# Kernel tuning notes

Hardware: AMD Instinct MI355X
Metric: run time of the kernel (lower is better)

## Reference

```python
import jax, jax.numpy as jnp
import numpy as np

A = 9          # num anchors per location
C = 256        # feature channels
H = W = 32     # feature map size
B = 1          # batch (module's squeeze_-based NMS implies batch=1)
N = A * H * W  # total proposals
IOU_THR = 0.9
EPS = 1e-5     # BatchNorm eps
NEG_SLOPE = 0.01  # LeakyReLU default


def setup_inputs() -> dict:
    key = jax.random.key(0)
    ks = jax.random.split(key, 8)
    inp = {
        "x": jax.random.normal(ks[0], (B, C, H, W), dtype=jnp.float32),
        "anchors": jax.random.uniform(ks[1], (A, 4), dtype=jnp.float32),
        # depthwise 3x3 conv (groups=C): torch weight shape [C,1,3,3]
        "dw_w": jax.random.normal(ks[2], (C, 1, 3, 3), dtype=jnp.float32) * 0.05,
        # pointwise 1x1 conv [C_out, C_in]
        "pw_w": jax.random.normal(ks[3], (C, C), dtype=jnp.float32) * 0.05,
        "bn1_gamma": jnp.ones((C,), jnp.float32),
        "bn1_beta": jnp.zeros((C,), jnp.float32),
        "bn1_mean": jnp.zeros((C,), jnp.float32),
        "bn1_var": jnp.ones((C,), jnp.float32),
        # anchors_conv: 1x1 conv 256 -> 4A, BN, ReLU6
        "anc_w": jax.random.normal(ks[4], (4 * A, C), dtype=jnp.float32) * 0.05,
        "anc_gamma": jnp.ones((4 * A,), jnp.float32),
        "anc_beta": jnp.zeros((4 * A,), jnp.float32),
        "anc_mean": jnp.zeros((4 * A,), jnp.float32),
        "anc_var": jnp.ones((4 * A,), jnp.float32),
        # objectness_conv: 1x1 conv 256 -> A, BN, Sigmoid
        "obj_w": jax.random.normal(ks[5], (A, C), dtype=jnp.float32) * 0.05,
        "obj_gamma": jnp.ones((A,), jnp.float32),
        "obj_beta": jnp.zeros((A,), jnp.float32),
        "obj_mean": jnp.zeros((A,), jnp.float32),
        "obj_var": jnp.ones((A,), jnp.float32),
    }
    return inp


def _bn(h, gamma, beta, mean, var):
    # inference-mode BatchNorm2d over channel dim 1 of [B,C,H,W]
    inv = jax.lax.rsqrt(var + EPS)
    return (h - mean[None, :, None, None]) * (inv * gamma)[None, :, None, None] + beta[None, :, None, None]


def _nms_keep(boxes, scores, thr):
    # greedy NMS (torchvision semantics, boxes as x1,y1,x2,y2) -> bool keep mask in original order
    order = jnp.argsort(-scores)
    b = boxes[order]  # [N,4] sorted by score desc
    x1, y1, x2, y2 = b[:, 0], b[:, 1], b[:, 2], b[:, 3]
    areas = (x2 - x1) * (y2 - y1)
    ix1 = jnp.maximum(x1[:, None], x1[None, :])
    iy1 = jnp.maximum(y1[:, None], y1[None, :])
    ix2 = jnp.minimum(x2[:, None], x2[None, :])
    iy2 = jnp.minimum(y2[:, None], y2[None, :])
    inter = jnp.clip(ix2 - ix1, 0.0) * jnp.clip(iy2 - iy1, 0.0)
    iou = inter / (areas[:, None] + areas[None, :] - inter)
    idx = jnp.arange(boxes.shape[0])

    def body(i, keep):
        sup = (iou[i] > thr) & (idx > i) & keep[i]
        return keep & ~sup

    keep_sorted = jax.lax.fori_loop(0, boxes.shape[0], body, jnp.ones((boxes.shape[0],), bool))
    return jnp.zeros((boxes.shape[0],), bool).at[order].set(keep_sorted)


def reference(x, anchors, dw_w, pw_w, bn1_gamma, bn1_beta, bn1_mean, bn1_var,
              anc_w, anc_gamma, anc_beta, anc_mean, anc_var,
              obj_w, obj_gamma, obj_beta, obj_mean, obj_var):
    batch = x.shape[0]
    hw = x.shape[2] * x.shape[3]
    # DepthSeparableConv2d: depthwise 3x3 (groups=C) + pointwise 1x1
    h = jax.lax.conv_general_dilated(
        x, dw_w, window_strides=(1, 1), padding=((1, 1), (1, 1)),
        dimension_numbers=("NCHW", "OIHW", "NCHW"), feature_group_count=C)
    h = jnp.einsum("bchw,oc->bohw", h, pw_w)
    h = jax.nn.leaky_relu(_bn(h, bn1_gamma, bn1_beta, bn1_mean, bn1_var), NEG_SLOPE)
    # heads
    anc = jnp.einsum("bchw,oc->bohw", h, anc_w)
    anc = jnp.clip(_bn(anc, anc_gamma, anc_beta, anc_mean, anc_var), 0.0, 6.0)  # ReLU6
    obj = jnp.einsum("bchw,oc->bohw", h, obj_w)
    obj = jax.nn.sigmoid(_bn(obj, obj_gamma, obj_beta, obj_mean, obj_var))
    # anchor decode
    corr = anc.reshape(batch, A, 4, hw)              # [B,A,4,HW]
    anch = anchors.reshape(1, A, 4, 1)
    pos = corr[:, :, :2, :] + anch[:, :, :2, :]
    size = jnp.exp(corr[:, :, 2:, :]) * anch[:, :, 2:, :]
    corrected = jnp.concatenate([pos, size], axis=2)  # [B,A,4,HW]
    boxes = corrected.transpose(0, 2, 1, 3).reshape(batch, 4, -1).transpose(0, 2, 1)  # [B,N,4]
    scores = obj.reshape(batch, A, 1, hw).transpose(0, 2, 1, 3).reshape(batch, 1, -1).transpose(0, 2, 1)  # [B,N,1]
    boxes = boxes[0]          # squeeze_ (batch==1)
    scores = scores[0, :, 0]
    keep = _nms_keep(boxes, scores, IOU_THR)
    m = jax.lax.stop_gradient(keep.astype(boxes.dtype))
    # fixed-shape equivalent of index_select: suppressed rows zeroed
    return jnp.concatenate([boxes * m[:, None], (scores * m)[:, None]], axis=1)  # [N,5]
```

## Files before the change

kernel.cpp:

```cpp
#include <hip/hip_runtime.h>
#include <hip/hip_bf16.h>

#define EPSF 1e-5f
#define IOU_THRF 0.9f
#define NBOX 9216
#define NWORDS 144
#define CAND_CAP 4096
#define FIRE_CAP 1024
#define NTILES 666

__global__ __launch_bounds__(256) void dw_conv(const float* __restrict__ x,
                                               const float* __restrict__ w,
                                               float* __restrict__ h0) {
    int idx = blockIdx.x * 256 + threadIdx.x;
    int c = idx >> 10, p = idx & 1023;
    int yy = p >> 5, xx = p & 31;
    const float* xi = x + (c << 10);
    const float* wc = w + c * 9;
    float acc = 0.f;
    #pragma unroll
    for (int dy = -1; dy <= 1; ++dy) {
        int y2 = yy + dy;
        if ((unsigned)y2 >= 32u) continue;
        #pragma unroll
        for (int dx = -1; dx <= 1; ++dx) {
            int x2 = xx + dx;
            if ((unsigned)x2 >= 32u) continue;
            acc += wc[(dy + 1) * 3 + (dx + 1)] * xi[y2 * 32 + x2];
        }
    }
    h0[idx] = acc;
}

__global__ __launch_bounds__(256) void pw_conv(const float* __restrict__ h0,
                                               const float* __restrict__ w,
                                               const float* __restrict__ g,
                                               const float* __restrict__ b,
                                               const float* __restrict__ mu,
                                               const float* __restrict__ var,
                                               float* __restrict__ h1) {
    int p = blockIdx.x * 256 + threadIdx.x;
    int o0 = blockIdx.y * 4;
    float acc0 = 0.f, acc1 = 0.f, acc2 = 0.f, acc3 = 0.f;
    for (int c = 0; c < 256; ++c) {
        float hv = h0[(c << 10) + p];
        acc0 += w[(o0 + 0) * 256 + c] * hv;
        acc1 += w[(o0 + 1) * 256 + c] * hv;
        acc2 += w[(o0 + 2) * 256 + c] * hv;
        acc3 += w[(o0 + 3) * 256 + c] * hv;
    }
    float accs[4] = {acc0, acc1, acc2, acc3};
    #pragma unroll
    for (int k = 0; k < 4; ++k) {
        int o = o0 + k;
        float inv = 1.0f / sqrtf(var[o] + EPSF);
        float v = (accs[k] - mu[o]) * (inv * g[o]) + b[o];
        v = (v >= 0.f) ? v : 0.01f * v;
        h1[(o << 10) + p] = v;
    }
}

__global__ __launch_bounds__(256) void heads(const float* __restrict__ h1,
                                             const float* __restrict__ anc_w,
                                             const float* __restrict__ ag,
                                             const float* __restrict__ ab,
                                             const float* __restrict__ am,
                                             const float* __restrict__ av,
                                             const float* __restrict__ obj_w,
                                             const float* __restrict__ og,
                                             const float* __restrict__ ob,
                                             const float* __restrict__ om,
                                             const float* __restrict__ ov,
                                             const float* __restrict__ anchors,
                                             float* __restrict__ boxes,
                                             float* __restrict__ scores) {
    int p = blockIdx.x * 256 + threadIdx.x;
    int o = blockIdx.y;
    const float* wrow = (o < 36) ? (anc_w + o * 256) : (obj_w + (o - 36) * 256);
    float acc = 0.f;
    for (int c = 0; c < 256; ++c) acc += wrow[c] * h1[(c << 10) + p];
    if (o < 36) {
        float inv = 1.0f / sqrtf(av[o] + EPSF);
        float v = (acc - am[o]) * (inv * ag[o]) + ab[o];
        v = fminf(fmaxf(v, 0.f), 6.f);
        int a = o >> 2, k = o & 3;
        float anch = anchors[a * 4 + k];
        float val = (k < 2) ? (v + anch) : (expf(v) * anch);
        boxes[(size_t)(a * 1024 + p) * 4 + k] = val;
    } else {
        int a = o - 36;
        float inv = 1.0f / sqrtf(ov[a] + EPSF);
        float v = (acc - om[a]) * (inv * og[a]) + ob[a];
        scores[a * 1024 + p] = 1.0f / (1.0f + expf(-v));
    }
}

__global__ __launch_bounds__(256) void rank_partial(const float* __restrict__ scores,
                                                    unsigned* __restrict__ rank) {
    __shared__ float4 sm[288];
    int mbase = blockIdx.y * 1152;
    for (int t = threadIdx.x; t < 288; t += 256)
        sm[t] = ((const float4*)(scores + mbase))[t];
    __syncthreads();
    int n = blockIdx.x * 256 + threadIdx.x;
    float s = scores[n];
    unsigned cnt = 0;
    for (int q = 0; q < 288; ++q) {
        float4 v = sm[q];
        int m = mbase + q * 4;
        cnt += (v.x > s) || (v.x == s && (m + 0) < n);
        cnt += (v.y > s) || (v.y == s && (m + 1) < n);
        cnt += (v.z > s) || (v.z == s && (m + 2) < n);
        cnt += (v.w > s) || (v.w == s && (m + 3) < n);
    }
    atomicAdd(&rank[n], cnt);
}

__global__ __launch_bounds__(256) void scatter_sorted(const float* __restrict__ boxes,
                                                      const unsigned* __restrict__ rank,
                                                      int* __restrict__ order,
                                                      float* __restrict__ sboxes,
                                                      float* __restrict__ sareas) {
    int n = blockIdx.x * 256 + threadIdx.x;
    unsigned r = rank[n];
    order[r] = n;
    float4 bx = ((const float4*)boxes)[n];
    ((float4*)sboxes)[r] = bx;
    sareas[r] = (bx.z - bx.x) * (bx.w - bx.y);
}

__global__ __launch_bounds__(256) void cand_detect(const float* __restrict__ sboxes,
                                                   const float* __restrict__ sareas,
                                                   unsigned long long* __restrict__ rnz64) {
    __shared__ float CX1[256], CY1[256], CX2[256], CY2[256], CAR[256];
    int rem = blockIdx.x, rb = 0;
    while (rem >= 36 - rb) { rem -= 36 - rb; ++rb; }
    int s = rb + rem;
    int tid = threadIdx.x;
    int i = rb * 256 + tid;
    {
        int j = s * 256 + tid;
        float4 cb = ((const float4*)sboxes)[j];
        CX1[tid] = cb.x; CY1[tid] = cb.y; CX2[tid] = cb.z; CY2[tid] = cb.w;
        CAR[tid] = sareas[j];
    }
    __syncthreads();
    float4 b = ((const float4*)sboxes)[i];
    float ar = sareas[i];
    bool any = false;

    if (s == rb) {
        for (int idx = tid + 1; idx < 256; ++idx) {
            float ix = fminf(b.z, CX2[idx]) - fmaxf(b.x, CX1[idx]);
            float iy = fminf(b.w, CY2[idx]) - fmaxf(b.y, CY1[idx]);
            float inter = fmaxf(ix, 0.f) * fmaxf(iy, 0.f);
            float denom = ar + CAR[idx] - inter;
            if (inter > 0.85f * denom) {
                if (inter / denom > IOU_THRF) any = true;
            }
        }
    } else {
        const float4* X1v = (const float4*)CX1;
        const float4* Y1v = (const float4*)CY1;
        const float4* X2v = (const float4*)CX2;
        const float4* Y2v = (const float4*)CY2;
        const float4* ARv = (const float4*)CAR;
        #pragma unroll 2
        for (int q = 0; q < 64; ++q) {
            float4 x1 = X1v[q], y1 = Y1v[q], x2 = X2v[q], y2 = Y2v[q], aa = ARv[q];
            #define CCHK(k) { \
                float ix = fminf(b.z, x2.k) - fmaxf(b.x, x1.k); \
                float iy = fminf(b.w, y2.k) - fmaxf(b.y, y1.k); \
                float inter = fmaxf(ix, 0.f) * fmaxf(iy, 0.f);  \
                float denom = ar + aa.k - inter;                \
                if (inter > 0.85f * denom) {                    \
                    if (inter / denom > IOU_THRF) any = true;   \
                } }
            CCHK(x) CCHK(y) CCHK(z) CCHK(w)
            #undef CCHK
        }
    }
    unsigned long long bal = __ballot(any);
    if ((tid & 63) == 0) atomicOr(&rnz64[rb * 4 + (tid >> 6)], bal);
}

__global__ __launch_bounds__(64) void compact_cand(const unsigned long long* __restrict__ rnz64,
                                                   const float* __restrict__ sboxes,
                                                   const float* __restrict__ sareas,
                                                   int* __restrict__ cidx,
                                                   float4* __restrict__ cboxes,
                                                   float* __restrict__ carea,
                                                   int* __restrict__ knum) {
    int lane = threadIdx.x;
    int base = 0;
    for (int w = 0; w < NWORDS; ++w) {
        unsigned long long bits = rnz64[w];
        if (bits & (1ull << lane)) {
            int pos = base + (int)__popcll(bits & ((1ull << lane) - 1ull));
            if (pos < CAND_CAP) {
                int i = w * 64 + lane;
                cidx[pos] = i;
                cboxes[pos] = ((const float4*)sboxes)[i];
                carea[pos] = sareas[i];
            }
        }
        base += (int)__popcll(bits);
    }
    if (lane == 0) knum[0] = base < CAND_CAP ? base : CAND_CAP;
}

__global__ __launch_bounds__(256) void gate_build(const float4* __restrict__ cboxes,
                                                  const float* __restrict__ carea,
                                                  const int* __restrict__ knum,
                                                  unsigned long long* __restrict__ gate) {
    int Kc = knum[0];
    int a = blockIdx.x * 4 + (threadIdx.x >> 6);
    int w = threadIdx.x & 63;
    if (a >= Kc) return;
    float4 b = cboxes[a];
    float ar = carea[a];
    unsigned long long bits = 0ull;
    int cbase = w * 64;
    if (cbase < Kc) {
        int lim = Kc - cbase; if (lim > 64) lim = 64;
        for (int t = 0; t < lim; ++t) {
            int c = cbase + t;
            if (c > a) {
                float4 cb = cboxes[c];
                float ix = fminf(b.z, cb.z) - fmaxf(b.x, cb.x);
                float iy = fminf(b.w, cb.w) - fmaxf(b.y, cb.y);
                float inter = fmaxf(ix, 0.f) * fmaxf(iy, 0.f);
                float denom = ar + carea[c] - inter;
                if (inter > 0.85f * denom) {
                    if (inter / denom > IOU_THRF) bits |= (1ull << t);
                }
            }
        }
    }
    gate[(size_t)a * 64 + w] = bits;
}

__device__ inline unsigned long long rdl64(unsigned long long v, int l) {
    unsigned lo = (unsigned)__builtin_amdgcn_readlane((int)(unsigned)(v & 0xffffffffull), l);
    unsigned hi = (unsigned)__builtin_amdgcn_readlane((int)(unsigned)(v >> 32), l);
    return ((unsigned long long)hi << 32) | lo;
}

__global__ __launch_bounds__(64) void nms_scan2(const unsigned long long* __restrict__ gate,
                                                const int* __restrict__ knum,
                                                int* __restrict__ fire_ord,
                                                int* __restrict__ fire_cnt) {
    int lane = threadIdx.x;
    int Kc = knum[0];
    int nw = (Kc + 63) >> 6;
    unsigned long long sup = 0ull;
    int nf = 0;
    for (int w = 0; w < nw; ++w) {
        int rem = Kc - w * 64;
        unsigned long long mskw = (rem >= 64) ? ~0ull : ((1ull << rem) - 1ull);
        unsigned long long alive = ~rdl64(sup, w) & mskw;
        while (alive) {
            unsigned long long snap = alive;
            int t0 = __builtin_ctzll(snap); snap &= snap - 1;
            int t1 = -1, t2 = -1, t3 = -1, t4 = -1, t5 = -1, t6 = -1, t7 = -1;
            if (snap) { t1 = __builtin_ctzll(snap); snap &= snap - 1; }
            if (snap) { t2 = __builtin_ctzll(snap); snap &= snap - 1; }
            if (snap) { t3 = __builtin_ctzll(snap); snap &= snap - 1; }
            if (snap) { t4 = __builtin_ctzll(snap); snap &= snap - 1; }
            if (snap) { t5 = __builtin_ctzll(snap); snap &= snap - 1; }
            if (snap) { t6 = __builtin_ctzll(snap); snap &= snap - 1; }
            if (snap) { t7 = __builtin_ctzll(snap); snap &= snap - 1; }
            int u1 = t1 < 0 ? t0 : t1, u2 = t2 < 0 ? t0 : t2, u3 = t3 < 0 ? t0 : t3;
            int u4 = t4 < 0 ? t0 : t4, u5 = t5 < 0 ? t0 : t5, u6 = t6 < 0 ? t0 : t6;
            int u7 = t7 < 0 ? t0 : t7;
            size_t wb = (size_t)(w << 6);
            unsigned long long g0 = gate[(wb + t0) * 64 + lane];
            unsigned long long g1 = gate[(wb + u1) * 64 + lane];
            unsigned long long g2 = gate[(wb + u2) * 64 + lane];
            unsigned long long g3 = gate[(wb + u3) * 64 + lane];
            unsigned long long g4 = gate[(wb + u4) * 64 + lane];
            unsigned long long g5 = gate[(wb + u5) * 64 + lane];
            unsigned long long g6 = gate[(wb + u6) * 64 + lane];
            unsigned long long g7 = gate[(wb + u7) * 64 + lane];
            #define PROC(tk, gk) \
                if (tk >= 0 && ((alive >> tk) & 1ull)) { \
                    if (lane == 0 && nf < FIRE_CAP) fire_ord[nf] = (w << 6) + tk; \
                    ++nf; sup |= gk; \
                    alive &= ~(1ull << tk); \
                    alive &= ~rdl64(gk, w); \
                }
            PROC(t0, g0) PROC(t1, g1) PROC(t2, g2) PROC(t3, g3)
            PROC(t4, g4) PROC(t5, g5) PROC(t6, g6) PROC(t7, g7)
            #undef PROC
        }
    }
    if (lane == 0) fire_cnt[0] = nf < FIRE_CAP ? nf : FIRE_CAP;
}

__global__ __launch_bounds__(256) void finalize(const float* __restrict__ sboxes,
                                                const float* __restrict__ sareas,
                                                const float* __restrict__ scores,
                                                const int* __restrict__ order,
                                                const float4* __restrict__ cboxes,
                                                const float* __restrict__ carea,
                                                const int* __restrict__ cidx,
                                                const int* __restrict__ fire_ord,
                                                const int* __restrict__ fire_cnt,
                                                float* __restrict__ out) {
    __shared__ float4 FB[FIRE_CAP];
    __shared__ float FA[FIRE_CAP];
    __shared__ int FP[FIRE_CAP];
    int tid = threadIdx.x;
    int fc = fire_cnt[0];
    for (int k = tid; k < fc; k += 256) {
        int o = fire_ord[k];
        FB[k] = cboxes[o];
        FA[k] = carea[o];
        FP[k] = cidx[o];
    }
    __syncthreads();
    int j = blockIdx.x * 256 + tid;
    float4 b = ((const float4*)sboxes)[j];
    float aj = sareas[j];
    bool supp = false;
    for (int k = 0; k < fc; ++k) {
        float4 f = FB[k];
        float ix = fminf(b.z, f.z) - fmaxf(b.x, f.x);
        float iy = fminf(b.w, f.w) - fmaxf(b.y, f.y);
        float inter = fmaxf(ix, 0.f) * fmaxf(iy, 0.f);
        float denom = FA[k] + aj - inter;
        if (FP[k] < j && inter > 0.85f * denom) {
            if (inter / denom > IOU_THRF) supp = true;
        }
    }
    int n = order[j];
    float m = supp ? 0.f : 1.f;
    out[(size_t)n * 5 + 0] = b.x * m;
    out[(size_t)n * 5 + 1] = b.y * m;
    out[(size_t)n * 5 + 2] = b.z * m;
    out[(size_t)n * 5 + 3] = b.w * m;
    out[(size_t)n * 5 + 4] = scores[n] * m;
}

extern "C" void kernel_launch(void* const* d_in, const int* in_sizes, int n_in,
                              void* d_out, int out_size, void* d_ws, size_t ws_size,
                              hipStream_t stream) {
    const float* x      = (const float*)d_in[0];
    const float* anchors= (const float*)d_in[1];
    const float* dw_w   = (const float*)d_in[2];
    const float* pw_w   = (const float*)d_in[3];
    const float* bn1g   = (const float*)d_in[4];
    const float* bn1b   = (const float*)d_in[5];
    const float* bn1m   = (const float*)d_in[6];
    const float* bn1v   = (const float*)d_in[7];
    const float* anc_w  = (const float*)d_in[8];
    const float* ag     = (const float*)d_in[9];
    const float* ab     = (const float*)d_in[10];
    const float* am     = (const float*)d_in[11];
    const float* av     = (const float*)d_in[12];
    const float* obj_w  = (const float*)d_in[13];
    const float* og     = (const float*)d_in[14];
    const float* ob     = (const float*)d_in[15];
    const float* om     = (const float*)d_in[16];
    const float* ov     = (const float*)d_in[17];
    float* out = (float*)d_out;

    char* ws = (char*)d_ws;
    size_t off = 0;
    auto alloc = [&](size_t bytes) -> char* {
        char* p = ws + off;
        off = (off + bytes + 255) & ~(size_t)255;
        return p;
    };
    float* h0      = (float*)alloc(256 * 1024 * 4);
    float* h1      = (float*)alloc(256 * 1024 * 4);
    float* boxes   = (float*)alloc(NBOX * 4 * 4);
    float* scores  = (float*)alloc(NBOX * 4);
    unsigned* rank = (unsigned*)alloc(NBOX * 4);
    int* order     = (int*)alloc(NBOX * 4);
    float* sboxes  = (float*)alloc(NBOX * 4 * 4);
    float* sareas  = (float*)alloc(NBOX * 4);
    unsigned long long* rnz64 = (unsigned long long*)alloc(NWORDS * 8);
    int* cidx      = (int*)alloc(CAND_CAP * 4);
    float4* cboxes = (float4*)alloc(CAND_CAP * 16);
    float* carea   = (float*)alloc(CAND_CAP * 4);
    int* knum      = (int*)alloc(256);
    int* fire_ord  = (int*)alloc(FIRE_CAP * 4);
    int* fire_cnt  = (int*)alloc(256);
    unsigned long long* gate = (unsigned long long*)alloc((size_t)CAND_CAP * 64 * 8);

    hipMemsetAsync(rank, 0, NBOX * 4, stream);
    hipMemsetAsync(rnz64, 0, NWORDS * 8, stream);

    dw_conv<<<1024, 256, 0, stream>>>(x, dw_w, h0);
    pw_conv<<<dim3(4, 64), 256, 0, stream>>>(h0, pw_w, bn1g, bn1b, bn1m, bn1v, h1);
    heads<<<dim3(4, 45), 256, 0, stream>>>(h1, anc_w, ag, ab, am, av,
                                           obj_w, og, ob, om, ov, anchors, boxes, scores);
    rank_partial<<<dim3(36, 8), 256, 0, stream>>>(scores, rank);
    scatter_sorted<<<36, 256, 0, stream>>>(boxes, rank, order, sboxes, sareas);
    cand_detect<<<NTILES, 256, 0, stream>>>(sboxes, sareas, rnz64);
    compact_cand<<<1, 64, 0, stream>>>(rnz64, sboxes, sareas, cidx, cboxes, carea, knum);
    gate_build<<<CAND_CAP / 4, 256, 0, stream>>>(cboxes, carea, knum, gate);
    nms_scan2<<<1, 64, 0, stream>>>(gate, knum, fire_ord, fire_cnt);
    finalize<<<36, 256, 0, stream>>>(sboxes, sareas, scores, order,
                                     cboxes, carea, cidx, fire_ord, fire_cnt, out);
}
```

Baseline: 366.5 us.

## Decouple serial NMS scan from gate loads using diagonal gate blocks and delayed suppression

gate_build now also writes the diagonal and next-diagonal 64-bit gate words per candidate into compact arrays. The serial single-wave scan reads these from registers (prefetched two words ahead) to resolve in-word and next-word suppression. This takes the dependent global gate load off the critical per-keep path. Full gate rows are queued and OR'd into the suppression mask two iterations later, so their load latency is hidden. compact_cand also loads the rnz64 bitmask once into registers and reads words via readlane instead of issuing a broadcast global load per word. The risks are added register pressure, branchy queue handling, and a subtle correctness dependence on the two-word delay.

Measured after the change: 445.7 us. 1.22x slower.

```diff
diff --git a/kernel.cpp b/kernel.cpp
--- a/kernel.cpp
+++ b/kernel.cpp
@@ -184,6 +184,12 @@
     if ((tid & 63) == 0) atomicOr(&rnz64[rb * 4 + (tid >> 6)], bal);
 }
 
+__device__ inline unsigned long long rdl64(unsigned long long v, int l) {
+    unsigned lo = (unsigned)__builtin_amdgcn_readlane((int)(unsigned)(v & 0xffffffffull), l);
+    unsigned hi = (unsigned)__builtin_amdgcn_readlane((int)(unsigned)(v >> 32), l);
+    return ((unsigned long long)hi << 32) | lo;
+}
+
 __global__ __launch_bounds__(64) void compact_cand(const unsigned long long* __restrict__ rnz64,
                                                    const float* __restrict__ sboxes,
                                                    const float* __restrict__ sareas,
@@ -192,9 +198,13 @@
                                                    float* __restrict__ carea,
                                                    int* __restrict__ knum) {
     int lane = threadIdx.x;
+    unsigned long long rz0 = rnz64[lane];
+    unsigned long long rz1 = rnz64[64 + lane];
+    unsigned long long rz2 = rnz64[128 + lane];
     int base = 0;
     for (int w = 0; w < NWORDS; ++w) {
-        unsigned long long bits = rnz64[w];
+        unsigned long long bits = (w < 64) ? rdl64(rz0, w)
+                                : (w < 128) ? rdl64(rz1, w - 64) : rdl64(rz2, w - 128);
         if (bits & (1ull << lane)) {
             int pos = base + (int)__popcll(bits & ((1ull << lane) - 1ull));
             if (pos < CAND_CAP) {
@@ -212,7 +222,9 @@
 __global__ __launch_bounds__(256) void gate_build(const float4* __restrict__ cboxes,
                                                   const float* __restrict__ carea,
                                                   const int* __restrict__ knum,
-                                                  unsigned long long* __restrict__ gate) {
+                                                  unsigned long long* __restrict__ gate,
+                                                  unsigned long long* __restrict__ diag0,
+                                                  unsigned long long* __restrict__ diag1) {
     int Kc = knum[0];
     int a = blockIdx.x * 4 + (threadIdx.x >> 6);
     int w = threadIdx.x & 63;
@@ -238,15 +250,14 @@
         }
     }
     gate[(size_t)a * 64 + w] = bits;
-}
-
-__device__ inline unsigned long long rdl64(unsigned long long v, int l) {
-    unsigned lo = (unsigned)__builtin_amdgcn_readlane((int)(unsigned)(v & 0xffffffffull), l);
-    unsigned hi = (unsigned)__builtin_amdgcn_readlane((int)(unsigned)(v >> 32), l);
-    return ((unsigned long long)hi << 32) | lo;
+    int aw = a >> 6;
+    if (w == aw) diag0[a] = bits;
+    if (w == aw + 1) diag1[a] = bits;
 }
 
 __global__ __launch_bounds__(64) void nms_scan2(const unsigned long long* __restrict__ gate,
+                                                const unsigned long long* __restrict__ diag0,
+                                                const unsigned long long* __restrict__ diag1,
                                                 const int* __restrict__ knum,
                                                 int* __restrict__ fire_ord,
                                                 int* __restrict__ fire_cnt) {
@@ -254,45 +265,48 @@
     int Kc = knum[0];
     int nw = (Kc + 63) >> 6;
     unsigned long long sup = 0ull;
+    unsigned long long carry = 0ull;
     int nf = 0;
+
+    unsigned long long qa0=0,qa1=0,qa2=0,qa3=0,qa4=0,qa5=0,qa6=0,qa7=0; int nA = 0;
+    unsigned long long qb0=0,qb1=0,qb2=0,qb3=0,qb4=0,qb5=0,qb6=0,qb7=0; int nB = 0;
+
+    unsigned long long d0A = diag0[lane], d0B = diag0[64 + lane];
+    unsigned long long d1A = diag1[lane], d1B = diag1[64 + lane];
+
     for (int w = 0; w < nw; ++w) {
-        int rem = Kc - w * 64;
-        unsigned long long mskw = (rem >= 64) ? ~0ull : ((1ull << rem) - 1ull);
-        unsigned long long alive = ~rdl64(sup, w) & mskw;
+        int pf = (w + 2) * 64 + lane;
+        unsigned long long d0C = diag0[pf];
+        unsigned long long d1C = diag1[pf];
+
+        if (nB > 0) { sup |= qb0;
+            if (nB > 1) sup |= qb1; if (nB > 2) sup |= qb2; if (nB > 3) sup |= qb3;
+            if (nB > 4) sup |= qb4; if (nB > 5) sup |= qb5; if (nB > 6) sup |= qb6;
+            if (nB > 7) sup |= qb7; }
+        qb0=qa0; qb1=qa1; qb2=qa2; qb3=qa3; qb4=qa4; qb5=qa5; qb6=qa6; qb7=qa7;
+        nB = nA; nA = 0;
+
+        int rem = Kc - (w << 6);
+        unsigned long long maskw = (rem >= 64) ? ~0ull : ((1ull << rem) - 1ull);
+        unsigned long long alive = ~(rdl64(sup, w) | carry) & maskw;
+        unsigned long long carry_next = 0ull;
+
         while (alive) {
-            unsigned long long snap = alive;
-            int t0 = __builtin_ctzll(snap); snap &= snap - 1;
-            int t1 = -1, t2 = -1, t3 = -1, t4 = -1, t5 = -1, t6 = -1, t7 = -1;
-            if (snap) { t1 = __builtin_ctzll(snap); snap &= snap - 1; }
-            if (snap) { t2 = __builtin_ctzll(snap); snap &= snap - 1; }
-            if (snap) { t3 = __builtin_ctzll(snap); snap &= snap - 1; }
-            if (snap) { t4 = __builtin_ctzll(snap); snap &= snap - 1; }
-            if (snap) { t5 = __builtin_ctzll(snap); snap &= snap - 1; }
-            if (snap) { t6 = __builtin_ctzll(snap); snap &= snap - 1; }
-            if (snap) { t7 = __builtin_ctzll(snap); snap &= snap - 1; }
-            int u1 = t1 < 0 ? t0 : t1, u2 = t2 < 0 ? t0 : t2, u3 = t3 < 0 ? t0 : t3;
-            int u4 = t4 < 0 ? t0 : t4, u5 = t5 < 0 ? t0 : t5, u6 = t6 < 0 ? t0 : t6;
-            int u7 = t7 < 0 ? t0 : t7;
-            size_t wb = (size_t)(w << 6);
-            unsigned long long g0 = gate[(wb + t0) * 64 + lane];
-            unsigned long long g1 = gate[(wb + u1) * 64 + lane];
-            unsigned long long g2 = gate[(wb + u2) * 64 + lane];
-            unsigned long long g3 = gate[(wb + u3) * 64 + lane];
-            unsigned long long g4 = gate[(wb + u4) * 64 + lane];
-            unsigned long long g5 = gate[(wb + u5) * 64 + lane];
-            unsigned long long g6 = gate[(wb + u6) * 64 + lane];
-            unsigned long long g7 = gate[(wb + u7) * 64 + lane];
-            #define PROC(tk, gk) \
-                if (tk >= 0 && ((alive >> tk) & 1ull)) { \
-                    if (lane == 0 && nf < FIRE_CAP) fire_ord[nf] = (w << 6) + tk; \
-                    ++nf; sup |= gk; \
-                    alive &= ~(1ull << tk); \
-                    alive &= ~rdl64(gk, w); \
-                }
-            PROC(t0, g0) PROC(t1, g1) PROC(t2, g2) PROC(t3, g3)
-            PROC(t4, g4) PROC(t5, g5) PROC(t6, g6) PROC(t7, g7)
-            #undef PROC
-        }
+            int t = __builtin_ctzll(alive);
+            if (lane == 0 && nf < FIRE_CAP) fire_ord[nf] = (w << 6) + t;
+            ++nf;
+            unsigned long long g = gate[((size_t)(w << 6) + t) * 64 + lane];
+            if (nA == 0) qa0 = g; else if (nA == 1) qa1 = g; else if (nA == 2) qa2 = g;
+            else if (nA == 3) qa3 = g; else if (nA == 4) qa4 = g; else if (nA == 5) qa5 = g;
+            else if (nA == 6) qa6 = g; else if (nA == 7) qa7 = g;
+            else sup |= g;
+            if (nA < 8) ++nA;
+            alive &= ~(1ull << t);
+            alive &= ~rdl64(d0A, t);
+            carry_next |= rdl64(d1A, t);
+        }
+        carry = carry_next;
+        d0A = d0B; d0B = d0C; d1A = d1B; d1B = d1C;
     }
     if (lane == 0) fire_cnt[0] = nf < FIRE_CAP ? nf : FIRE_CAP;
 }
@@ -380,17 +394,19 @@
     int* order     = (int*)alloc(NBOX * 4);
     float* sboxes  = (float*)alloc(NBOX * 4 * 4);
     float* sareas  = (float*)alloc(NBOX * 4);
-    unsigned long long* rnz64 = (unsigned long long*)alloc(NWORDS * 8);
+    unsigned long long* rnz64 = (unsigned long long*)alloc(192 * 8);
     int* cidx      = (int*)alloc(CAND_CAP * 4);
     float4* cboxes = (float4*)alloc(CAND_CAP * 16);
     float* carea   = (float*)alloc(CAND_CAP * 4);
     int* knum      = (int*)alloc(256);
     int* fire_ord  = (int*)alloc(FIRE_CAP * 4);
     int* fire_cnt  = (int*)alloc(256);
-    unsigned long long* gate = (unsigned long long*)alloc((size_t)CAND_CAP * 64 * 8);
+    unsigned long long* gate  = (unsigned long long*)alloc((size_t)CAND_CAP * 64 * 8);
+    unsigned long long* diag0 = (unsigned long long*)alloc((CAND_CAP + 192) * 8);
+    unsigned long long* diag1 = (unsigned long long*)alloc((CAND_CAP + 192) * 8);
 
     hipMemsetAsync(rank, 0, NBOX * 4, stream);
-    hipMemsetAsync(rnz64, 0, NWORDS * 8, stream);
+    hipMemsetAsync(rnz64, 0, 192 * 8, stream);
 
     dw_conv<<<1024, 256, 0, stream>>>(x, dw_w, h0);
     pw_conv<<<dim3(4, 64), 256, 0, stream>>>(h0, pw_w, bn1g, bn1b, bn1m, bn1v, h1);
@@ -400,8 +416,8 @@
     scatter_sorted<<<36, 256, 0, stream>>>(boxes, rank, order, sboxes, sareas);
     cand_detect<<<NTILES, 256, 0, stream>>>(sboxes, sareas, rnz64);
     compact_cand<<<1, 64, 0, stream>>>(rnz64, sboxes, sareas, cidx, cboxes, carea, knum);
-    gate_build<<<CAND_CAP / 4, 256, 0, stream>>>(cboxes, carea, knum, gate);
-    nms_scan2<<<1, 64, 0, stream>>>(gate, knum, fire_ord, fire_cnt);
+    gate_build<<<CAND_CAP / 4, 256, 0, stream>>>(cboxes, carea, knum, gate, diag0, diag1);
+    nms_scan2<<<1, 64, 0, stream>>>(gate, diag0, diag1, knum, fire_ord, fire_cnt);
     finalize<<<36, 256, 0, stream>>>(sboxes, sareas, scores, order,
                                      cboxes, carea, cidx, fire_ord, fire_cnt, out);
 }
```
